# Kernel optimization log

Measured on AMD Instinct MI355X. Metric: run time of the kernel, lower is better.

## Reference

```python
import jax, jax.numpy as jnp
import numpy as np
from jax import lax

BINS = 16
N_FFT = 2 * (BINS - 1)  # 30


def setup_inputs() -> dict:
    key = jax.random.key(0)
    k0, k1, k2, k3 = jax.random.split(key, 4)
    B, C, T = 16, 256, 8192
    c = C // BINS  # 16
    s = 1.0 / np.sqrt(C)  # keep attention logits in a sane range
    return {
        "x": jax.random.normal(k0, (B, C, T), dtype=jnp.float32),
        "Wk": jax.random.normal(k1, (c, C), dtype=jnp.float32) * s,
        "Wq": jax.random.normal(k2, (C, C), dtype=jnp.float32) * s,
        "Wv": jax.random.normal(k3, (C, C), dtype=jnp.float32) * s,
    }


def _spectrogram_power(sig):
    """torchaudio T.Spectrogram(n_fft=30, hop_length=1, normalized=True, power=2),
    implemented as a direct windowed-DFT conv (exact same math as the FFT).
    sig: [N, L] -> [N, BINS, L+1] frames (center=True, reflect pad)."""
    n = jnp.arange(N_FFT, dtype=jnp.float32)
    window = 0.5 - 0.5 * jnp.cos(2.0 * np.pi * n / N_FFT)  # periodic Hann
    kf = jnp.arange(BINS, dtype=jnp.float32)
    ang = 2.0 * np.pi * kf[:, None] * n[None, :] / N_FFT  # [BINS, N_FFT]
    # real and imaginary DFT kernels, window folded in: [2*BINS, N_FFT]
    dft = jnp.concatenate([jnp.cos(ang), -jnp.sin(ang)], axis=0) * window
    pad = N_FFT // 2
    sigp = jnp.pad(sig, ((0, 0), (pad, pad)), mode="reflect")[:, None, :]  # [N,1,L+30]
    spec = lax.conv_general_dilated(
        sigp, dft[:, None, :].astype(sig.dtype), (1,), "VALID",
        dimension_numbers=("NCH", "OIH", "NCH"))  # [N, 2*BINS, L+1]
    power = spec[:, :BINS, :] ** 2 + spec[:, BINS:, :] ** 2
    return power / jnp.sum(window ** 2)  # normalized=True -> / ||w||^2 on power


def reference(x, Wk, Wq, Wv):
    B, C, T = x.shape
    c = Wk.shape[0]
    xt = x.transpose(0, 2, 1)  # [B, T, C]
    k = jnp.einsum("btC,cC->bct", xt, Wk)   # [B, c, T]
    q = jnp.einsum("btC,cC->bct", xt, Wq)   # [B, C, T]
    v = jnp.einsum("btC,cC->bct", xt, Wv)   # [B, C, T]
    scores = jnp.einsum("bct,bCt->bcC", k, q) / (C ** 0.5)
    scores = jax.nn.softmax(scores, axis=-1)           # [B, c, C]
    out = jnp.einsum("bCt,bcC->bct", v, scores)        # [B, c, T]
    power = _spectrogram_power(out.reshape(B * c, T))  # [B*c, BINS, T+1]
    power = power[..., :T]                             # drop last frame ([:-1])
    return power.reshape(B, c * BINS, T)
```

## Files before the change

### kernel.cpp

```cpp
#include <hip/hip_runtime.h>
#include <math.h>

#define B_   16
#define C_   256
#define T_   8192
#define BINS 16
#define NFFT 30

typedef __attribute__((ext_vector_type(8))) _Float16 f16x8;
typedef __attribute__((ext_vector_type(2))) __fp16 fp16x2;
typedef __attribute__((ext_vector_type(4))) float f32x4;

typedef const __attribute__((address_space(1))) unsigned int ga_u32;
typedef __attribute__((address_space(3))) unsigned int ls_u32;

union f16pack { f16x8 v; fp16x2 p[4]; };

__global__ __launch_bounds__(512) void spec_tables(float* __restrict__ ctab,
                                                   float* __restrict__ stab) {
  const int i = threadIdx.x;
  if (i < BINS*NFFT) {
    const int k = i / NFFT, n = i % NFFT;
    const float TWO_PI = 6.283185307179586f;
    const float wn = 0.5f - 0.5f * cosf(TWO_PI * (float)n / (float)NFFT);
    const float ang = TWO_PI * (float)(k * n) / (float)NFFT;
    ctab[i] = cosf(ang) * wn;
    stab[i] = sinf(ang) * wn;
  }
}

__global__ __launch_bounds__(256) void k_kernel(const float* __restrict__ x,
                                                const float* __restrict__ Wk,
                                                _Float16* __restrict__ kk) {
  const int tc = blockIdx.x;
  const int b  = blockIdx.y;
  const int tid = threadIdx.x;
  const int t = tc*256 + tid;
  const float* xb = x + (size_t)b*C_*T_ + t;
  float acc[16];
#pragma unroll
  for (int cc = 0; cc < 16; ++cc) acc[cc] = 0.f;
  for (int c4 = 0; c4 < 64; ++c4) {
    float xv[4];
#pragma unroll
    for (int j = 0; j < 4; ++j) xv[j] = xb[(size_t)(c4*4 + j)*T_];
#pragma unroll
    for (int cc = 0; cc < 16; ++cc) {
      const float4 w4 = *(const float4*)&Wk[cc*256 + c4*4];
      acc[cc] += w4.x*xv[0] + w4.y*xv[1] + w4.z*xv[2] + w4.w*xv[3];
    }
  }
#pragma unroll
  for (int cc = 0; cc < 16; ++cc)
    kk[((size_t)b*16 + cc)*T_ + t] = (_Float16)acc[cc];
}

static __device__ __forceinline__ void stage_panel(float* dstbase, const float* xb,
                                                   int koff, int tid) {
#pragma unroll
  for (int h = 0; h < 4; ++h) {
    const int idx = h*512 + tid;
    const int row = idx >> 3;
    const int ps  = idx & 7;
    const int ls  = ps ^ (row & 7);
    const float* src = xb + (size_t)row*T_ + koff + ls*4;
    __builtin_amdgcn_global_load_lds((ga_u32*)src, (ls_u32*)(dstbase + idx*4), 16, 0, 0);
  }
}

__global__ __launch_bounds__(512, 4) void r_kernel(const float* __restrict__ x,
                                                   const _Float16* __restrict__ kk,
                                                   float* __restrict__ Rp) {
  const int ks = blockIdx.x;
  const int b  = blockIdx.y;
  constexpr int KCH = 256;

  __shared__ float P[2][256*32];

  const int tid  = threadIdx.x;
  const int lane = tid & 63;
  const int w    = tid >> 6;
  const int fr   = lane & 15;
  const int g    = lane >> 4;

  const float* xb = x + (size_t)b*C_*T_;
  const _Float16* kb = kk + (size_t)b*16*T_;
  const int t0 = ks * KCH;

  f32x4 acc[2];
  acc[0] = (f32x4){0.f,0.f,0.f,0.f};
  acc[1] = (f32x4){0.f,0.f,0.f,0.f};

  stage_panel(P[0], xb, t0, tid);
  __syncthreads();

  int cur = 0;
  for (int kt = 0; kt < KCH; kt += 32) {
    if (kt + 32 < KCH) stage_panel(P[cur ^ 1], xb, t0 + kt + 32, tid);

    const float* Pc = P[cur];
    const f16x8 ka = *(const f16x8*)&kb[(size_t)fr*T_ + t0 + kt + g*8];
#pragma unroll
    for (int nt = 0; nt < 2; ++nt) {
      const int r = (w*2 + nt)*16 + fr;
      const float4 lo = *(const float4*)&Pc[r*32 + (((2*g+0) ^ (r&7))<<2)];
      const float4 hi = *(const float4*)&Pc[r*32 + (((2*g+1) ^ (r&7))<<2)];
      f16pack fb;
      fb.p[0] = __builtin_amdgcn_cvt_pkrtz(lo.x, lo.y);
      fb.p[1] = __builtin_amdgcn_cvt_pkrtz(lo.z, lo.w);
      fb.p[2] = __builtin_amdgcn_cvt_pkrtz(hi.x, hi.y);
      fb.p[3] = __builtin_amdgcn_cvt_pkrtz(hi.z, hi.w);
      acc[nt] = __builtin_amdgcn_mfma_f32_16x16x32_f16(ka, fb.v, acc[nt], 0, 0, 0);
    }
    __syncthreads();
    cur ^= 1;
  }

  float* rp = Rp + ((size_t)(ks*16 + b))*4096;
#pragma unroll
  for (int nt = 0; nt < 2; ++nt)
#pragma unroll
    for (int r = 0; r < 4; ++r) {
      const int cc = g*4 + r;
      const int ch = (w*2 + nt)*16 + fr;
      rp[cc*256 + ch] = acc[nt][r];
    }
}

__global__ __launch_bounds__(256) void reduce_kernel(const float* __restrict__ Rp,
                                                     float* __restrict__ wkg) {
  const int idx = blockIdx.x*256 + threadIdx.x;
  const int b   = idx >> 12;
  const int rem = idx & 4095;
  float s = 0.f;
#pragma unroll 8
  for (int p = 0; p < 32; ++p)
    s += Rp[((size_t)(p*16 + b))*4096 + rem];
  wkg[idx] = s;
}

__global__ __launch_bounds__(256) void attn_b(const float* __restrict__ Wq,
                                              const float* __restrict__ Wv,
                                              const float* __restrict__ wkg,
                                              float* __restrict__ Mout) {
  const int b = blockIdx.x;
  const int tid = threadIdx.x;
  __shared__ float s1[16*256];
  __shared__ float s2[16*256];
  __shared__ float invs[16];

#pragma unroll
  for (int cc = 0; cc < 16; ++cc) s1[cc*256 + tid] = wkg[(size_t)b*4096 + cc*256 + tid];
  __syncthreads();

  float sc[16];
#pragma unroll
  for (int cc = 0; cc < 16; ++cc) sc[cc] = 0.f;
  for (int c4 = 0; c4 < 64; ++c4) {
    const float4 wq4 = *(const float4*)&Wq[(size_t)tid*256 + c4*4];
#pragma unroll
    for (int cc = 0; cc < 16; ++cc) {
      const float4 p4 = *(const float4*)&s1[cc*256 + c4*4];
      sc[cc] += p4.x*wq4.x + p4.y*wq4.y + p4.z*wq4.z + p4.w*wq4.w;
    }
  }
#pragma unroll
  for (int cc = 0; cc < 16; ++cc) s2[cc*256 + tid] = sc[cc] * 0.0625f;
  __syncthreads();

  {
    const int rr = tid >> 4, jj = tid & 15;
    float mx = -1e30f;
    for (int c = jj; c < 256; c += 16) mx = fmaxf(mx, s2[rr*256 + c]);
    for (int o = 1; o < 16; o <<= 1) mx = fmaxf(mx, __shfl_xor(mx, o, 64));
    float sm = 0.f;
    for (int c = jj; c < 256; c += 16) {
      const float e = __expf(s2[rr*256 + c] - mx);
      s2[rr*256 + c] = e;
      sm += e;
    }
    for (int o = 1; o < 16; o <<= 1) sm += __shfl_xor(sm, o, 64);
    if (jj == 0) invs[rr] = 1.f / sm;
  }
  __syncthreads();

  float mac[16];
#pragma unroll
  for (int cc = 0; cc < 16; ++cc) mac[cc] = 0.f;
  for (int c4 = 0; c4 < 64; ++c4) {
    float wv[4];
#pragma unroll
    for (int j = 0; j < 4; ++j) wv[j] = Wv[(size_t)(c4*4 + j)*256 + tid];
#pragma unroll
    for (int cc = 0; cc < 16; ++cc) {
      const float4 p4 = *(const float4*)&s2[cc*256 + c4*4];
      mac[cc] += p4.x*wv[0] + p4.y*wv[1] + p4.z*wv[2] + p4.w*wv[3];
    }
  }
#pragma unroll
  for (int cc = 0; cc < 16; ++cc)
    Mout[(size_t)b*4096 + cc*256 + tid] = mac[cc] * invs[cc];
}

__global__ __launch_bounds__(256) void outp_kernel(const float* __restrict__ x,
                                                   const float* __restrict__ M,
                                                   float* __restrict__ seq) {
  const int tc = blockIdx.x;
  const int b  = blockIdx.y;
  const int tid = threadIdx.x;
  const int t  = tc*512 + tid*2;
  const float* xb = x + (size_t)b*C_*T_ + t;
  const float* mb = M + (size_t)b*4096;
  float2 a[16];
#pragma unroll
  for (int cc = 0; cc < 16; ++cc) a[cc] = make_float2(0.f, 0.f);
  for (int ch = 0; ch < 64; ++ch) {
    float2 xv[4];
#pragma unroll
    for (int j = 0; j < 4; ++j)
      xv[j] = *(const float2*)(xb + (size_t)(ch*4 + j) * T_);
#pragma unroll
    for (int cc = 0; cc < 16; ++cc) {
      const float4 m4 = *(const float4*)(mb + cc*256 + ch*4);
      a[cc].x += m4.x*xv[0].x + m4.y*xv[1].x + m4.z*xv[2].x + m4.w*xv[3].x;
      a[cc].y += m4.x*xv[0].y + m4.y*xv[1].y + m4.z*xv[2].y + m4.w*xv[3].y;
    }
  }
#pragma unroll
  for (int cc = 0; cc < 16; ++cc)
    *(float2*)(seq + (size_t)(b*16 + cc)*T_ + t) = a[cc];
}

__global__ __launch_bounds__(256) void spec_kernel(const float* __restrict__ seq,
                                                   const float* __restrict__ ctabg,
                                                   const float* __restrict__ stabg,
                                                   float* __restrict__ out) {
  const int tcx = blockIdx.x;
  const int r   = blockIdx.y;
  const int tid = threadIdx.x;
  const int t0  = tcx * 256;

  __shared__ float smem[288];
  __shared__ float ctab[BINS*NFFT];
  __shared__ float stab[BINS*NFFT];

  const float* row = seq + (size_t)r * T_;
  for (int i = tid; i < 288; i += 256) {
    int gg = t0 - 15 + i;
    if (gg < 0) gg = -gg;
    if (gg > T_-1) gg = 2*(T_-1) - gg;
    smem[i] = row[gg];
  }
  for (int i = tid; i < BINS*NFFT; i += 256) {
    ctab[i] = ctabg[i];
    stab[i] = stabg[i];
  }
  __syncthreads();

  const int k   = tid >> 4;
  const int sub = tid & 15;
  float cr[NFFT], ci[NFFT];
#pragma unroll
  for (int n = 0; n < NFFT; ++n) { cr[n] = ctab[k*NFFT + n]; ci[n] = stab[k*NFFT + n]; }

  float* orow = out + (size_t)(r*BINS + k) * T_ + t0;
  const float inv_norm = 1.0f / 11.25f;

  for (int jj = 0; jj < 4; ++jj) {
    const int x0 = 4*sub + 64*jj;
    float smp[36];
#pragma unroll
    for (int q = 0; q < 9; ++q) {
      const float4 v = *(const float4*)&smem[x0 + 4*q];
      smp[4*q+0] = v.x; smp[4*q+1] = v.y; smp[4*q+2] = v.z; smp[4*q+3] = v.w;
    }
    float4 pw;
#pragma unroll
    for (int p = 0; p < 4; ++p) {
      float re = 0.f, im = 0.f;
#pragma unroll
      for (int n = 0; n < NFFT; ++n) {
        re += cr[n] * smp[p + n];
        im += ci[n] * smp[p + n];
      }
      ((float*)&pw)[p] = (re*re + im*im) * inv_norm;
    }
    *(float4*)(orow + x0) = pw;
  }
}

extern "C" void kernel_launch(void* const* d_in, const int* in_sizes, int n_in,
                              void* d_out, int out_size, void* d_ws, size_t ws_size,
                              hipStream_t stream) {
  const float* x  = (const float*)d_in[0];
  const float* Wk = (const float*)d_in[1];
  const float* Wq = (const float*)d_in[2];
  const float* Wv = (const float*)d_in[3];
  float* out = (float*)d_out;
  float* ws  = (float*)d_ws;

  _Float16* kk = (_Float16*)ws;
  float* Rp   = ws + 1048576;
  float* wkg  = Rp + 2097152;
  float* M    = wkg + 65536;
  float* seq  = M + 65536;
  float* ctab = seq + 2097152;
  float* stab = ctab + 480;

  spec_tables<<<1, 512, 0, stream>>>(ctab, stab);
  k_kernel<<<dim3(32, 16), 256, 0, stream>>>(x, Wk, kk);
  r_kernel<<<dim3(32, 16), 512, 0, stream>>>(x, kk, Rp);
  reduce_kernel<<<dim3(256), 256, 0, stream>>>(Rp, wkg);
  attn_b<<<dim3(16), 256, 0, stream>>>(Wq, Wv, wkg, M);
  outp_kernel<<<dim3(16, 16), 256, 0, stream>>>(x, M, seq);
  spec_kernel<<<dim3(32, 256), 256, 0, stream>>>(seq, ctab, stab, out);
}
```

Measured before the change: 216.3 us.

## Drop table kernel, widen k_kernel to two timesteps, split attn_b across 512 threads

Removes the separate spec_tables launch and computes the windowed DFT tables inside each spec_kernel block, saving one launch at the cost of redundant trig work per block. k_kernel now processes two timesteps per thread with float2 loads and packed fp16 stores, halving its grid. attn_b uses 512 threads, each handling 8 of the 16 rows, to raise parallelism in the single-wave-per-batch attention step. These are separate tweaks to launch count, vector width and thread parallelism.

Measured after the change: 213.5 us (median of 2 runs). Within noise of the previous version (-1.3%).

```diff
diff --git a/kernel.cpp b/kernel.cpp
--- a/kernel.cpp
+++ b/kernel.cpp
@@ -15,19 +15,6 @@
 typedef __attribute__((address_space(3))) unsigned int ls_u32;
 
 union f16pack { f16x8 v; fp16x2 p[4]; };
-
-__global__ __launch_bounds__(512) void spec_tables(float* __restrict__ ctab,
-                                                   float* __restrict__ stab) {
-  const int i = threadIdx.x;
-  if (i < BINS*NFFT) {
-    const int k = i / NFFT, n = i % NFFT;
-    const float TWO_PI = 6.283185307179586f;
-    const float wn = 0.5f - 0.5f * cosf(TWO_PI * (float)n / (float)NFFT);
-    const float ang = TWO_PI * (float)(k * n) / (float)NFFT;
-    ctab[i] = cosf(ang) * wn;
-    stab[i] = sinf(ang) * wn;
-  }
-}
 
 __global__ __launch_bounds__(256) void k_kernel(const float* __restrict__ x,
                                                 const float* __restrict__ Wk,
@@ -35,24 +22,29 @@
   const int tc = blockIdx.x;
   const int b  = blockIdx.y;
   const int tid = threadIdx.x;
-  const int t = tc*256 + tid;
+  const int t = tc*512 + tid*2;
   const float* xb = x + (size_t)b*C_*T_ + t;
-  float acc[16];
-#pragma unroll
-  for (int cc = 0; cc < 16; ++cc) acc[cc] = 0.f;
+  float2 acc[16];
+#pragma unroll
+  for (int cc = 0; cc < 16; ++cc) acc[cc] = make_float2(0.f, 0.f);
   for (int c4 = 0; c4 < 64; ++c4) {
-    float xv[4];
-#pragma unroll
-    for (int j = 0; j < 4; ++j) xv[j] = xb[(size_t)(c4*4 + j)*T_];
+    float2 xv[4];
+#pragma unroll
+    for (int j = 0; j < 4; ++j) xv[j] = *(const float2*)(xb + (size_t)(c4*4 + j)*T_);
 #pragma unroll
     for (int cc = 0; cc < 16; ++cc) {
       const float4 w4 = *(const float4*)&Wk[cc*256 + c4*4];
-      acc[cc] += w4.x*xv[0] + w4.y*xv[1] + w4.z*xv[2] + w4.w*xv[3];
-    }
-  }
-#pragma unroll
-  for (int cc = 0; cc < 16; ++cc)
-    kk[((size_t)b*16 + cc)*T_ + t] = (_Float16)acc[cc];
+      acc[cc].x += w4.x*xv[0].x + w4.y*xv[1].x + w4.z*xv[2].x + w4.w*xv[3].x;
+      acc[cc].y += w4.x*xv[0].y + w4.y*xv[1].y + w4.z*xv[2].y + w4.w*xv[3].y;
+    }
+  }
+#pragma unroll
+  for (int cc = 0; cc < 16; ++cc) {
+    fp16x2 hv;
+    hv[0] = (__fp16)acc[cc].x;
+    hv[1] = (__fp16)acc[cc].y;
+    *(fp16x2*)&kk[((size_t)b*16 + cc)*T_ + t] = hv;
+  }
 }
 
 static __device__ __forceinline__ void stage_panel(float* dstbase, const float* xb,
@@ -139,7 +131,7 @@
   wkg[idx] = s;
 }
 
-__global__ __launch_bounds__(256) void attn_b(const float* __restrict__ Wq,
+__global__ __launch_bounds__(512) void attn_b(const float* __restrict__ Wq,
                                               const float* __restrict__ Wv,
                                               const float* __restrict__ wkg,
                                               float* __restrict__ Mout) {
@@ -149,57 +141,61 @@
   __shared__ float s2[16*256];
   __shared__ float invs[16];
 
-#pragma unroll
-  for (int cc = 0; cc < 16; ++cc) s1[cc*256 + tid] = wkg[(size_t)b*4096 + cc*256 + tid];
-  __syncthreads();
-
-  float sc[16];
-#pragma unroll
-  for (int cc = 0; cc < 16; ++cc) sc[cc] = 0.f;
+  for (int i = tid; i < 4096; i += 512) s1[i] = wkg[(size_t)b*4096 + i];
+  __syncthreads();
+
+  const int h   = tid >> 8;
+  const int col = tid & 255;
+
+  float sc[8];
+#pragma unroll
+  for (int i = 0; i < 8; ++i) sc[i] = 0.f;
   for (int c4 = 0; c4 < 64; ++c4) {
-    const float4 wq4 = *(const float4*)&Wq[(size_t)tid*256 + c4*4];
-#pragma unroll
-    for (int cc = 0; cc < 16; ++cc) {
-      const float4 p4 = *(const float4*)&s1[cc*256 + c4*4];
-      sc[cc] += p4.x*wq4.x + p4.y*wq4.y + p4.z*wq4.z + p4.w*wq4.w;
-    }
-  }
-#pragma unroll
-  for (int cc = 0; cc < 16; ++cc) s2[cc*256 + tid] = sc[cc] * 0.0625f;
+    const float4 wq4 = *(const float4*)&Wq[(size_t)col*256 + c4*4];
+#pragma unroll
+    for (int i = 0; i < 8; ++i) {
+      const float4 p4 = *(const float4*)&s1[(h*8 + i)*256 + c4*4];
+      sc[i] += p4.x*wq4.x + p4.y*wq4.y + p4.z*wq4.z + p4.w*wq4.w;
+    }
+  }
+#pragma unroll
+  for (int i = 0; i < 8; ++i) s2[(h*8 + i)*256 + col] = sc[i] * 0.0625f;
   __syncthreads();
 
   {
-    const int rr = tid >> 4, jj = tid & 15;
+    const int rr = tid >> 5, jj = tid & 31;
     float mx = -1e30f;
-    for (int c = jj; c < 256; c += 16) mx = fmaxf(mx, s2[rr*256 + c]);
-    for (int o = 1; o < 16; o <<= 1) mx = fmaxf(mx, __shfl_xor(mx, o, 64));
+    for (int c = jj; c < 256; c += 32) mx = fmaxf(mx, s2[rr*256 + c]);
+#pragma unroll
+    for (int o = 1; o < 32; o <<= 1) mx = fmaxf(mx, __shfl_xor(mx, o, 64));
     float sm = 0.f;
-    for (int c = jj; c < 256; c += 16) {
+    for (int c = jj; c < 256; c += 32) {
       const float e = __expf(s2[rr*256 + c] - mx);
       s2[rr*256 + c] = e;
       sm += e;
     }
-    for (int o = 1; o < 16; o <<= 1) sm += __shfl_xor(sm, o, 64);
+#pragma unroll
+    for (int o = 1; o < 32; o <<= 1) sm += __shfl_xor(sm, o, 64);
     if (jj == 0) invs[rr] = 1.f / sm;
   }
   __syncthreads();
 
-  float mac[16];
-#pragma unroll
-  for (int cc = 0; cc < 16; ++cc) mac[cc] = 0.f;
+  float mac[8];
+#pragma unroll
+  for (int i = 0; i < 8; ++i) mac[i] = 0.f;
   for (int c4 = 0; c4 < 64; ++c4) {
     float wv[4];
 #pragma unroll
-    for (int j = 0; j < 4; ++j) wv[j] = Wv[(size_t)(c4*4 + j)*256 + tid];
-#pragma unroll
-    for (int cc = 0; cc < 16; ++cc) {
-      const float4 p4 = *(const float4*)&s2[cc*256 + c4*4];
-      mac[cc] += p4.x*wv[0] + p4.y*wv[1] + p4.z*wv[2] + p4.w*wv[3];
-    }
-  }
-#pragma unroll
-  for (int cc = 0; cc < 16; ++cc)
-    Mout[(size_t)b*4096 + cc*256 + tid] = mac[cc] * invs[cc];
+    for (int j = 0; j < 4; ++j) wv[j] = Wv[(size_t)(c4*4 + j)*256 + col];
+#pragma unroll
+    for (int i = 0; i < 8; ++i) {
+      const float4 p4 = *(const float4*)&s2[(h*8 + i)*256 + c4*4];
+      mac[i] += p4.x*wv[0] + p4.y*wv[1] + p4.z*wv[2] + p4.w*wv[3];
+    }
+  }
+#pragma unroll
+  for (int i = 0; i < 8; ++i)
+    Mout[(size_t)b*4096 + (h*8 + i)*256 + col] = mac[i] * invs[h*8 + i];
 }
 
 __global__ __launch_bounds__(256) void outp_kernel(const float* __restrict__ x,
@@ -232,8 +228,6 @@
 }
 
 __global__ __launch_bounds__(256) void spec_kernel(const float* __restrict__ seq,
-                                                   const float* __restrict__ ctabg,
-                                                   const float* __restrict__ stabg,
                                                    float* __restrict__ out) {
   const int tcx = blockIdx.x;
   const int r   = blockIdx.y;
@@ -252,8 +246,12 @@
     smem[i] = row[gg];
   }
   for (int i = tid; i < BINS*NFFT; i += 256) {
-    ctab[i] = ctabg[i];
-    stab[i] = stabg[i];
+    const int k = i / NFFT, n = i % NFFT;
+    const float TWO_PI = 6.283185307179586f;
+    const float wn = 0.5f - 0.5f * cosf(TWO_PI * (float)n / (float)NFFT);
+    const float ang = TWO_PI * (float)(k * n) / (float)NFFT;
+    ctab[i] = cosf(ang) * wn;
+    stab[i] = sinf(ang) * wn;
   }
   __syncthreads();
 
@@ -304,14 +302,11 @@
   float* wkg  = Rp + 2097152;
   float* M    = wkg + 65536;
   float* seq  = M + 65536;
-  float* ctab = seq + 2097152;
-  float* stab = ctab + 480;
-
-  spec_tables<<<1, 512, 0, stream>>>(ctab, stab);
-  k_kernel<<<dim3(32, 16), 256, 0, stream>>>(x, Wk, kk);
+
+  k_kernel<<<dim3(16, 16), 256, 0, stream>>>(x, Wk, kk);
   r_kernel<<<dim3(32, 16), 512, 0, stream>>>(x, kk, Rp);
   reduce_kernel<<<dim3(256), 256, 0, stream>>>(Rp, wkg);
-  attn_b<<<dim3(16), 256, 0, stream>>>(Wq, Wv, wkg, M);
+  attn_b<<<dim3(16), 512, 0, stream>>>(Wq, Wv, wkg, M);
   outp_kernel<<<dim3(16, 16), 256, 0, stream>>>(x, M, seq);
-  spec_kernel<<<dim3(32, 256), 256, 0, stream>>>(seq, ctab, stab, out);
-}
+  spec_kernel<<<dim3(32, 256), 256, 0, stream>>>(seq, out);
+}
```
